# Kernel tuning notes

Measured on AMD Instinct MI355X. Metric: run time of the kernel, lower is better.

## Reference

```python
import jax, jax.numpy as jnp
from jax import lax
import numpy as np

# dims: batch, in_channels, out_channels, spatial, kernel, padding
B, IC, OC, H, W, K, PAD = 4, 64, 64, 32, 32, 3, 1


def setup_inputs() -> dict:
    key = jax.random.key(0)
    k1, k2, k3, k4 = jax.random.split(key, 4)
    # x is a binary (+/-1) activation in this stochastic binary network
    x = jnp.sign(jax.random.normal(k1, (B, IC, H, W), jnp.float32))
    x = jnp.where(x == 0, 1.0, x)
    # q: small per-unit correction probabilities
    q = jax.random.uniform(k2, (B, IC, H, W), jnp.float32) * 1e-3
    # xavier_uniform with sigmoid gain (=1.0), as in _reset_parameters
    fan_in, fan_out = IC * K * K, OC * K * K
    bound = float(np.sqrt(6.0 / (fan_in + fan_out)))
    weight = jax.random.uniform(k3, (OC, IC, K, K), jnp.float32, -bound, bound)
    bbound = float(1.0 / np.sqrt(fan_in))
    bias = jax.random.uniform(k4, (OC,), jnp.float32, -bbound, bbound)
    return {"x": x, "q": q, "weight": weight, "bias": bias}


def _forward(x, q, weight, bias, key):
    pad = 2 * (K // 2) - PAD  # = 1 for k=3, padding=1
    # a0 = conv(x), NCHW / OIHW
    a0 = lax.conv_general_dilated(x, weight, (1, 1), [(PAD, PAD), (PAD, PAD)]) \
         + bias[None, :, None, None]                      # [B,OC,H,W]
    p0 = jax.nn.sigmoid(a0)
    # stochastic binary sample new_x in {-1,+1}; sample is non-differentiable
    new_x = 2.0 * jax.random.bernoulli(key, p0).astype(p0.dtype) - 1.0

    Kf = jnp.flip(weight, (2, 3))                         # flipped kernel
    a0_ = jnp.pad(a0, ((0, 0), (0, 0), (pad, pad), (pad, pad)))     # [B,OC,H+K-1,W+K-1]
    p0_ = jnp.pad(p0, ((0, 0), (0, 0), (pad, pad), (pad, pad)))
    y_ = jnp.pad(new_x, ((0, 0), (0, 0), (pad, pad), (pad, pad)))

    # Fused version of _compute_conv_diffs + _compute_delta_sum: instead of
    # materializing the full [K,K,B,OC,IC,H,W] tensor, process each (l1,l2)
    # shift (K*K = 9 static iterations), same math.
    delta_q = jnp.zeros((B, OC, H + K - 1, W + K - 1), p0.dtype)
    for l1 in range(K):
        for l2 in range(K):
            # a[l1,l2] : pre-activation if input bit (l1,l2) were flipped
            a_l = a0_[:, :, None, l1:l1 + H, l2:l2 + W] \
                  - 2.0 * x[:, None] * Kf[None, :, :, l1, l2, None, None]  # [B,OC,IC,H,W]
            p_l = jax.nn.sigmoid(a_l)
            add = jnp.sum((p_l - p0_[:, :, None, l1:l1 + H, l2:l2 + W]) * q[:, None],
                          axis=2) * (-y_[:, :, l1:l1 + H, l2:l2 + W])       # [B,OC,H,W]
            delta_q = delta_q.at[:, :, l1:l1 + H, l2:l2 + W].add(add)
    delta_q = delta_q[:, :, pad:-pad, pad:-pad]           # [B,OC,H,W]

    # delta_0: zero in value, carries gradient of p0 (straight-through trick)
    delta_0 = -new_x * (p0 - lax.stop_gradient(p0))
    qs = jnp.sum(q, axis=(1, 2, 3), keepdims=True)        # [B,1,1,1]
    new_q = delta_0 * (1.0 - qs) + delta_q
    # stride == 1 -> the [::stride] slicing is a no-op
    return new_x, new_q


def reference(x, q, weight, bias):
    return _forward(x, q, weight, bias, jax.random.key(42))
```

## Files before the change

### kernel.cpp

```cpp
#include <hip/hip_runtime.h>
#include <cstdint>


typedef __attribute__((ext_vector_type(4))) int   i32x4;
typedef __attribute__((ext_vector_type(8))) short s16x8;
typedef __attribute__((ext_vector_type(4))) float f32x4;

static constexpr int OFF_X8   = 0;
static constexpr int OFF_XQH  = 295936;
static constexpr int OFF_QH   = 887808;
static constexpr int OFF_WD   = 1479680;
static constexpr int OFF_WB   = 1627136;
static constexpr int OFF_W2B  = 1700864;
static constexpr int OFF_U    = 1774592;

__device__ __forceinline__ uint32_t rotl32(uint32_t v, int n) {
  return (v << n) | (v >> (32 - n));
}

__device__ __forceinline__ unsigned short f2bf(float f) {
  uint32_t u = __float_as_uint(f);
  uint32_t r = (u + 0x7FFFu + ((u >> 16) & 1u)) >> 16;
  return (unsigned short)r;
}

__global__ __launch_bounds__(256) void prep_kernel(
    const float* __restrict__ x, const float* __restrict__ q,
    const float* __restrict__ weight, char* __restrict__ ws) {
  int idx = blockIdx.x * 256 + threadIdx.x;

  if (idx < 295936) {
    int ic = idx & 63;
    int t  = idx >> 6;
    int wp = t % 34;
    int t2 = t / 34;
    int hp = t2 % 34;
    int b  = t2 / 34;
    float xv = 0.f, qv = 0.f;
    if (hp >= 1 && hp <= 32 && wp >= 1 && wp <= 32) {
      int src = ((b * 64 + ic) * 32 + (hp - 1)) * 32 + (wp - 1);
      xv = x[src];
      qv = q[src];
    }
    ((char*)(ws + OFF_X8))[idx] = (char)(int)xv;
    ((unsigned short*)(ws + OFF_XQH))[idx] = f2bf(xv * qv);
    ((unsigned short*)(ws + OFF_QH))[idx]  = f2bf(qv);
  } else if (idx < 295936 + 262144) {
    uint32_t j  = (uint32_t)(idx - 295936);
    uint32_t x0 = 0u, x1 = j;
    const uint32_t ks0 = 0u, ks1 = 42u, ks2 = 0x1BD11BDAu ^ 42u;
    x0 += ks0; x1 += ks1;
#define QR(rot) { x0 += x1; x1 = rotl32(x1, rot); x1 ^= x0; }
    QR(13) QR(15) QR(26) QR(6)
    x0 += ks1; x1 += ks2 + 1u;
    QR(17) QR(29) QR(16) QR(24)
    x0 += ks2; x1 += ks0 + 2u;
    QR(13) QR(15) QR(26) QR(6)
    x0 += ks0; x1 += ks1 + 3u;
    QR(17) QR(29) QR(16) QR(24)
    x0 += ks1; x1 += ks2 + 4u;
    QR(13) QR(15) QR(26) QR(6)
    x0 += ks2; x1 += ks0 + 5u;
#undef QR
    uint32_t bits = x0 ^ x1;
    ((float*)(ws + OFF_U))[j] = __uint_as_float((bits >> 9) | 0x3F800000u) - 1.0f;
  } else if (idx < 295936 + 262144 + 36864) {
    int k  = idx - (295936 + 262144);
    int ic = k & 63;
    int t  = k >> 6;
    int oc  = t & 63;
    int tap = t >> 6;
    int kh = tap / 3, kw = tap % 3;
    float Wv = weight[((oc * 64 + ic) * 3 + kh) * 3 + kw];
    long long wi = llrint((double)Wv * 2147483648.0);
    char* wd = ws + OFF_WD;
#pragma unroll
    for (int dig = 0; dig < 4; ++dig) {
      signed char d = (signed char)(wi & 0xFF);
      wd[dig * 36864 + k] = d;
      wi = (wi - (long long)d) >> 8;
    }
    ((unsigned short*)(ws + OFF_WB))[k]  = f2bf(Wv);
    ((unsigned short*)(ws + OFF_W2B))[k] = f2bf(Wv * Wv);
  }
}

__global__ __launch_bounds__(256) void main_kernel(
    const char* __restrict__ ws, const float* __restrict__ bias,
    float* __restrict__ out) {
  const char* x8            = ws + OFF_X8;
  const unsigned short* xqh = (const unsigned short*)(ws + OFF_XQH);
  const unsigned short* qh  = (const unsigned short*)(ws + OFF_QH);
  const char* wd            = ws + OFF_WD;
  const unsigned short* wb  = (const unsigned short*)(ws + OFF_WB);
  const unsigned short* w2b = (const unsigned short*)(ws + OFF_W2B);
  const float* u            = (const float*)(ws + OFF_U);

  const int b  = blockIdx.x >> 6;
  const int h  = (blockIdx.x >> 1) & 31;
  const int nt = blockIdx.x & 1;

  const int octile = threadIdx.x >> 6;
  const int lane   = threadIdx.x & 63;
  const int quad   = lane >> 4;
  const int l16    = lane & 15;

  i32x4 accI[4];
#pragma unroll
  for (int d = 0; d < 4; ++d) accI[d] = (i32x4){0, 0, 0, 0};
  f32x4 aC1 = {0.f, 0.f, 0.f, 0.f};
  f32x4 aC2 = {0.f, 0.f, 0.f, 0.f};

  const int aoff_i8 = (octile * 16 + l16) * 64 + quad * 16;
  const int aoff_bf = (octile * 16 + l16) * 64 + quad * 8;

#pragma unroll
  for (int kh = 0; kh < 3; ++kh) {
#pragma unroll
    for (int kw = 0; kw < 3; ++kw) {
      const int tap = kh * 3 + kw;
      i32x4 aI[4];
#pragma unroll
      for (int d = 0; d < 4; ++d)
        aI[d] = *(const i32x4*)(wd + d * 36864 + tap * 4096 + aoff_i8);
      s16x8 aW0 = *(const s16x8*)(wb  + tap * 4096 + aoff_bf);
      s16x8 aW1 = *(const s16x8*)(wb  + tap * 4096 + aoff_bf + 32);
      s16x8 aV0 = *(const s16x8*)(w2b + tap * 4096 + aoff_bf);
      s16x8 aV1 = *(const s16x8*)(w2b + tap * 4096 + aoff_bf + 32);
      const int pix = ((b * 34 + h + kh) * 34 + (nt * 16 + l16 + kw)) * 64;
      i32x4 bI  = *(const i32x4*)(x8 + pix + quad * 16);
      s16x8 bX0 = *(const s16x8*)(xqh + pix + quad * 8);
      s16x8 bX1 = *(const s16x8*)(xqh + pix + 32 + quad * 8);
      s16x8 bQ0 = *(const s16x8*)(qh  + pix + quad * 8);
      s16x8 bQ1 = *(const s16x8*)(qh  + pix + 32 + quad * 8);
#pragma unroll
      for (int d = 0; d < 4; ++d)
        accI[d] = __builtin_amdgcn_mfma_i32_16x16x64_i8(aI[d], bI, accI[d], 0, 0, 0);
      aC1 = __builtin_amdgcn_mfma_f32_16x16x32_bf16(aW0, bX0, aC1, 0, 0, 0);
      aC1 = __builtin_amdgcn_mfma_f32_16x16x32_bf16(aW1, bX1, aC1, 0, 0, 0);
      aC2 = __builtin_amdgcn_mfma_f32_16x16x32_bf16(aV0, bQ0, aC2, 0, 0, 0);
      aC2 = __builtin_amdgcn_mfma_f32_16x16x32_bf16(aV1, bQ1, aC2, 0, 0, 0);
    }
  }

  const int w = nt * 16 + l16;
#pragma unroll
  for (int r = 0; r < 4; ++r) {
    const int ocr = octile * 16 + quad * 4 + r;
    double a0 = (((double)accI[3][r] * 256.0 + (double)accI[2][r]) * 256.0 +
                 (double)accI[1][r]) * 256.0 + (double)accI[0][r];
    a0 = a0 * (1.0 / 2147483648.0) + (double)bias[ocr];
    double p0d = 1.0 / (1.0 + exp(-a0));
    const int o = ((b * 64 + ocr) * 32 + h) * 32 + w;
    float nx = ((double)u[o] < p0d) ? 1.0f : -1.0f;
    float p0 = (float)p0d;
    float s1 = p0 * (1.0f - p0);
    float s2 = s1 * (1.0f - 2.0f * p0);
    float dq = 2.0f * nx * (s1 * aC1[r] - s2 * aC2[r]);
    out[o] = nx;
    out[262144 + o] = dq;
  }
}

extern "C" void kernel_launch(void* const* d_in, const int* in_sizes, int n_in,
                              void* d_out, int out_size, void* d_ws, size_t ws_size,
                              hipStream_t stream) {
  const float* x      = (const float*)d_in[0];
  const float* q      = (const float*)d_in[1];
  const float* weight = (const float*)d_in[2];
  const float* bias   = (const float*)d_in[3];
  float* out = (float*)d_out;
  char* ws   = (char*)d_ws;

  prep_kernel<<<2324, 256, 0, stream>>>(x, q, weight, ws);
  main_kernel<<<256, 256, 0, stream>>>(ws, bias, out);
}
```

Baseline: 75.96 us.

## Inline Threefry sampling into main kernel and tile input repack through LDS

```diff
diff --git a/kernel.cpp b/kernel.cpp
--- a/kernel.cpp
+++ b/kernel.cpp
@@ -12,7 +12,6 @@
 static constexpr int OFF_WD   = 1479680;
 static constexpr int OFF_WB   = 1627136;
 static constexpr int OFF_W2B  = 1700864;
-static constexpr int OFF_U    = 1774592;
 
 __device__ __forceinline__ uint32_t rotl32(uint32_t v, int n) {
   return (v << n) | (v >> (32 - n));
@@ -24,48 +23,76 @@
   return (unsigned short)r;
 }
 
+__device__ __forceinline__ float threefry_u(uint32_t j) {
+  uint32_t x0 = 0u, x1 = j;
+  const uint32_t ks1 = 42u, ks2 = 0x1BD11BDAu ^ 42u;
+  x0 += 0u; x1 += ks1;
+#define QR(rot) { x0 += x1; x1 = rotl32(x1, rot); x1 ^= x0; }
+  QR(13) QR(15) QR(26) QR(6)
+  x0 += ks1; x1 += ks2 + 1u;
+  QR(17) QR(29) QR(16) QR(24)
+  x0 += ks2; x1 += 0u + 2u;
+  QR(13) QR(15) QR(26) QR(6)
+  x0 += 0u; x1 += ks1 + 3u;
+  QR(17) QR(29) QR(16) QR(24)
+  x0 += ks1; x1 += ks2 + 4u;
+  QR(13) QR(15) QR(26) QR(6)
+  x0 += ks2; x1 += 0u + 5u;
+#undef QR
+  uint32_t bits = x0 ^ x1;
+  return __uint_as_float((bits >> 9) | 0x3F800000u) - 1.0f;
+}
+
 __global__ __launch_bounds__(256) void prep_kernel(
     const float* __restrict__ x, const float* __restrict__ q,
     const float* __restrict__ weight, char* __restrict__ ws) {
-  int idx = blockIdx.x * 256 + threadIdx.x;
-
-  if (idx < 295936) {
-    int ic = idx & 63;
-    int t  = idx >> 6;
-    int wp = t % 34;
-    int t2 = t / 34;
-    int hp = t2 % 34;
-    int b  = t2 / 34;
-    float xv = 0.f, qv = 0.f;
-    if (hp >= 1 && hp <= 32 && wp >= 1 && wp <= 32) {
-      int src = ((b * 64 + ic) * 32 + (hp - 1)) * 32 + (wp - 1);
-      xv = x[src];
-      qv = q[src];
-    }
-    ((char*)(ws + OFF_X8))[idx] = (char)(int)xv;
-    ((unsigned short*)(ws + OFF_XQH))[idx] = f2bf(xv * qv);
-    ((unsigned short*)(ws + OFF_QH))[idx]  = f2bf(qv);
-  } else if (idx < 295936 + 262144) {
-    uint32_t j  = (uint32_t)(idx - 295936);
-    uint32_t x0 = 0u, x1 = j;
-    const uint32_t ks0 = 0u, ks1 = 42u, ks2 = 0x1BD11BDAu ^ 42u;
-    x0 += ks0; x1 += ks1;
-#define QR(rot) { x0 += x1; x1 = rotl32(x1, rot); x1 ^= x0; }
-    QR(13) QR(15) QR(26) QR(6)
-    x0 += ks1; x1 += ks2 + 1u;
-    QR(17) QR(29) QR(16) QR(24)
-    x0 += ks2; x1 += ks0 + 2u;
-    QR(13) QR(15) QR(26) QR(6)
-    x0 += ks0; x1 += ks1 + 3u;
-    QR(17) QR(29) QR(16) QR(24)
-    x0 += ks1; x1 += ks2 + 4u;
-    QR(13) QR(15) QR(26) QR(6)
-    x0 += ks2; x1 += ks0 + 5u;
-#undef QR
-    uint32_t bits = x0 ^ x1;
-    ((float*)(ws + OFF_U))[j] = __uint_as_float((bits >> 9) | 0x3F800000u) - 1.0f;
-  } else if (idx < 295936 + 262144 + 36864) {
-    int k  = idx - (295936 + 262144);
+  const int blk = blockIdx.x;
+  const int tid = threadIdx.x;
+
+  if (blk < 128) {
+    const int b = blk >> 5;
+    const int h = blk & 31;
+    __shared__ char           x8s[2048];
+    __shared__ unsigned short xqs[2048];
+    __shared__ unsigned short qs [2048];
+    const int ic = tid >> 2;
+    const int w0 = (tid & 3) * 8;
+    const int src = ((b * 64 + ic) * 32 + h) * 32 + w0;
+    float4 xa = *(const float4*)(x + src);
+    float4 xb = *(const float4*)(x + src + 4);
+    float4 qa = *(const float4*)(q + src);
+    float4 qb = *(const float4*)(q + src + 4);
+    float xv[8] = {xa.x, xa.y, xa.z, xa.w, xb.x, xb.y, xb.z, xb.w};
+    float qv[8] = {qa.x, qa.y, qa.z, qa.w, qb.x, qb.y, qb.z, qb.w};
+#pragma unroll
+    for (int j = 0; j < 8; ++j) {
+      int a = (w0 + j) * 64 + ic;
+      x8s[a] = (char)(int)xv[j];
+      xqs[a] = f2bf(xv[j] * qv[j]);
+      qs[a]  = f2bf(qv[j]);
+    }
+    __syncthreads();
+    const int rowel = ((b * 34 + h + 1) * 34 + 1) * 64;
+    ((uint2*)(ws + OFF_X8 + rowel))[tid]      = ((const uint2*)x8s)[tid];
+    ((uint4*)(ws + OFF_XQH + rowel * 2))[tid] = ((const uint4*)xqs)[tid];
+    ((uint4*)(ws + OFF_QH  + rowel * 2))[tid] = ((const uint4*)qs)[tid];
+  } else if (blk < 132) {
+    const int b = blk - 128;
+    for (int k = tid; k < 8448; k += 256) {
+      int cell = k >> 6;
+      int ic = k & 63;
+      int hp, wp;
+      if (cell < 34)       { hp = 0;          wp = cell; }
+      else if (cell < 68)  { hp = 33;         wp = cell - 34; }
+      else if (cell < 100) { hp = cell - 67;  wp = 0; }
+      else                 { hp = cell - 99;  wp = 33; }
+      int a = ((b * 34 + hp) * 34 + wp) * 64 + ic;
+      ((char*)(ws + OFF_X8))[a] = 0;
+      ((unsigned short*)(ws + OFF_XQH))[a] = 0;
+      ((unsigned short*)(ws + OFF_QH))[a]  = 0;
+    }
+  } else {
+    int k  = (blk - 132) * 256 + tid;
     int ic = k & 63;
     int t  = k >> 6;
     int oc  = t & 63;
@@ -94,7 +121,6 @@
   const char* wd            = ws + OFF_WD;
   const unsigned short* wb  = (const unsigned short*)(ws + OFF_WB);
   const unsigned short* w2b = (const unsigned short*)(ws + OFF_W2B);
-  const float* u            = (const float*)(ws + OFF_U);
 
   const int b  = blockIdx.x >> 6;
   const int h  = (blockIdx.x >> 1) & 31;
@@ -152,7 +178,8 @@
     a0 = a0 * (1.0 / 2147483648.0) + (double)bias[ocr];
     double p0d = 1.0 / (1.0 + exp(-a0));
     const int o = ((b * 64 + ocr) * 32 + h) * 32 + w;
-    float nx = ((double)u[o] < p0d) ? 1.0f : -1.0f;
+    float su = threefry_u((uint32_t)o);
+    float nx = ((double)su < p0d) ? 1.0f : -1.0f;
     float p0 = (float)p0d;
     float s1 = p0 * (1.0f - p0);
     float s2 = s1 * (1.0f - 2.0f * p0);
@@ -172,6 +199,6 @@
   float* out = (float*)d_out;
   char* ws   = (char*)d_ws;
 
-  prep_kernel<<<2324, 256, 0, stream>>>(x, q, weight, ws);
+  prep_kernel<<<276, 256, 0, stream>>>(x, q, weight, ws);
   main_kernel<<<256, 256, 0, stream>>>(ws, bias, out);
 }
```

Result: no change. 75.31 us (-0.8%).
